# Optimization experiments

Measured on AMD Instinct MI355X. Metric: run time of the kernel, lower is better.

The kernel has to match this reference:

```python
import jax, jax.numpy as jnp
import numpy as np

NUM_HEADS = 8
TAU = 2.0
BN_EPS = 1e-5


def _make_atan_spike(alpha):
    @jax.custom_vjp
    def spike(x):
        return (x >= 0.0).astype(x.dtype)
    def fwd(x):
        return spike(x), x
    def bwd(x, g):
        sg = (alpha / 2.0) / (1.0 + (jnp.pi / 2.0 * alpha * x) ** 2)
        return (g * sg,)
    spike.defvjp(fwd, bwd)
    return spike


def _make_sigmoid_spike(alpha):
    @jax.custom_vjp
    def spike(x):
        return (x >= 0.0).astype(x.dtype)
    def fwd(x):
        return spike(x), x
    def bwd(x, g):
        s = jax.nn.sigmoid(alpha * x)
        return (g * alpha * s * (1.0 - s),)
    spike.defvjp(fwd, bwd)
    return spike

_atan_spike = _make_atan_spike(5.0)       # surrogate.ATan(alpha=5.0)
_sigmoid_spike = _make_sigmoid_spike(4.0)  # spikingjelly default surrogate.Sigmoid(alpha=4.0)


def lif_multistep(x_seq, v_threshold, spike_fn):
    """Multi-step LIF, tau=2, hard reset to 0, detach_reset=True, decay_input=True.
    x_seq: [T, ...]. Returns spike sequence [T, ...]."""
    def step(v, x):
        h = v + (x - v) / TAU
        s = spike_fn(h - v_threshold)
        sd = jax.lax.stop_gradient(s)  # detach_reset
        v_new = h * (1.0 - sd)         # hard reset to v_reset=0
        return v_new, s
    _, s_seq = jax.lax.scan(step, jnp.zeros_like(x_seq[0]), x_seq)
    return s_seq


def bn(x, gamma, beta, mean, var):
    # inference-mode BatchNorm1d over channel dim C of [T,B,C,N]
    inv = gamma / jnp.sqrt(var + BN_EPS)
    return (x - mean[None, None, :, None]) * inv[None, None, :, None] + beta[None, None, :, None]


def setup_inputs() -> dict:
    key = jax.random.key(0)
    T, B, C, H, W = 4, 32, 384, 16, 16
    ks = jax.random.split(key, 20)
    d = {"x": jax.random.normal(ks[0], (T, B, C, H, W), dtype=jnp.float32)}
    std = 1.0 / np.sqrt(C)
    for i, p in enumerate(["q", "k", "proj"]):
        d[p + "_w"] = jax.random.normal(ks[1 + 5 * i], (C, C), dtype=jnp.float32) * std
        d[p + "_gamma"] = jnp.ones((C,), jnp.float32) + 0.1 * jax.random.normal(ks[2 + 5 * i], (C,))
        d[p + "_beta"] = 0.1 * jax.random.normal(ks[3 + 5 * i], (C,))
        d[p + "_mean"] = 0.1 * jax.random.normal(ks[4 + 5 * i], (C,))
        d[p + "_var"] = jax.random.uniform(ks[5 + 5 * i], (C,), minval=0.5, maxval=1.5)
    d["proj_b"] = 0.01 * jax.random.normal(ks[16], (C,))
    return d


def reference(x, q_w, q_gamma, q_beta, q_mean, q_var,
              k_w, k_gamma, k_beta, k_mean, k_var,
              proj_w, proj_gamma, proj_beta, proj_mean, proj_var, proj_b):
    T, B, C, H, W = x.shape
    N = H * W
    Ch = C // NUM_HEADS
    xf = x.reshape(T, B, C, N)

    # q branch: 1x1 conv (C x C matmul) -> BN -> LIF
    q = bn(jnp.einsum('tbcn,dc->tbdn', xf, q_w), q_gamma, q_beta, q_mean, q_var)
    q = lif_multistep(q, 1.0, _atan_spike)
    q = q.reshape(T, B, NUM_HEADS, Ch, N)
    q = jnp.sum(q, axis=3, keepdims=True)          # [T,B,h,1,N]
    attn = lif_multistep(q, 0.5, _sigmoid_spike)    # attn_lif, v_threshold=0.5

    # k branch
    k = bn(jnp.einsum('tbcn,dc->tbdn', xf, k_w), k_gamma, k_beta, k_mean, k_var)
    k = lif_multistep(k, 1.0, _atan_spike)
    k = k.reshape(T, B, NUM_HEADS, Ch, N)

    y = (attn * k).reshape(T, B, C, N)

    # proj: 1x1 conv with bias -> BN -> LIF
    y = jnp.einsum('tbcn,dc->tbdn', y, proj_w) + proj_b[None, None, :, None]
    y = bn(y, proj_gamma, proj_beta, proj_mean, proj_var)
    y = lif_multistep(y, 1.0, _atan_spike)
    return y.reshape(T, B, C, H, W)
```

## Files before the change

### kernel.cpp

```cpp
#include <hip/hip_runtime.h>

typedef _Float16 f16x8 __attribute__((ext_vector_type(8)));
typedef _Float16 f16x4 __attribute__((ext_vector_type(4)));
typedef float    f32x4 __attribute__((ext_vector_type(4)));

#define TT 4
#define BB 32
#define CC 384
#define NN 256

#define WS_X1   25165824
#define WS_WSP  50331648
#define WS_Y    52101120
#define WS_NEED 77266944

__device__ __forceinline__ void async16(void* lds, const void* g) {
    __builtin_amdgcn_global_load_lds(
        (const __attribute__((address_space(1))) unsigned int*)g,
        (__attribute__((address_space(3))) unsigned int*)lds, 16, 0, 0);
}

__global__ __launch_bounds__(256) void wprep(
    const float* __restrict__ qw, const float* __restrict__ kw,
    const float* __restrict__ pw, _Float16* __restrict__ wsp)
{
    int gid = blockIdx.x * 256 + threadIdx.x;
    int which = gid / 36864;
    int e4 = (gid % 36864) * 4;
    const float* src = (which == 0) ? qw : (which == 1) ? kw : pw;
    _Float16* d0 = wsp + (size_t)which * 294912;
    _Float16* d1 = d0 + 147456;
    float4 v = *(const float4*)(src + e4);
    f16x4 h0, h1;
    float vv[4] = {v.x, v.y, v.z, v.w};
#pragma unroll
    for (int j = 0; j < 4; ++j) {
        _Float16 a = (_Float16)vv[j];
        float r = vv[j] - (float)a;
        h0[j] = a; h1[j] = (_Float16)r;
    }
    *(f16x4*)(d0 + e4) = h0;
    *(f16x4*)(d1 + e4) = h1;
}

__global__ __launch_bounds__(256) void xprep(
    const float* __restrict__ x, _Float16* __restrict__ x0,
    _Float16* __restrict__ x1)
{
    __shared__ float xs[64 * 65];
    const int tid = threadIdx.x;
    int bid = blockIdx.x;
    int tb = bid / 24, r = bid % 24;
    int c0 = (r >> 2) * 64, n0 = (r & 3) * 64;

#pragma unroll
    for (int p = 0; p < 4; ++p) {
        int c = (tid >> 4) + p * 16;
        int nl = (tid & 15) * 4;
        float4 v = *(const float4*)&x[((size_t)tb * CC + c0 + c) * NN + n0 + nl];
        *(float4*)&xs[c * 65 + nl] = v;
    }
    __syncthreads();
    int n = tid >> 2, cg = (tid & 3) * 16;
#pragma unroll
    for (int j4 = 0; j4 < 4; ++j4) {
        int c = cg + j4 * 4;
        f16x4 h0, h1;
#pragma unroll
        for (int jj = 0; jj < 4; ++jj) {
            float v = xs[(c + jj) * 65 + n];
            _Float16 a = (_Float16)v;
            float rr = v - (float)a;
            h0[jj] = a; h1[jj] = (_Float16)rr;
        }
        size_t o = ((size_t)tb * NN + n0 + n) * CC + c0 + c;
        *(f16x4*)(x0 + o) = h0;
        *(f16x4*)(x1 + o) = h1;
    }
}

__global__ __launch_bounds__(256, 2) void qk_mfma(
    const _Float16* __restrict__ x0, const _Float16* __restrict__ x1,
    const _Float16* __restrict__ wsp,
    const float* __restrict__ qg, const float* __restrict__ qbe,
    const float* __restrict__ qm, const float* __restrict__ qva,
    const float* __restrict__ kg, const float* __restrict__ kbe,
    const float* __restrict__ km, const float* __restrict__ kva,
    _Float16* __restrict__ y)
{
    __shared__ __align__(16) _Float16 ldsW[12 * 512];

    const int tid  = threadIdx.x;
    const int wave = tid >> 6;
    const int lane = tid & 63;
    const int m16  = lane & 15;
    const int quad = lane >> 4;

    int bid = blockIdx.x;
    int r8 = bid & 7, u = bid >> 3;
    int head = u & 7;
    int s = ((u >> 3) << 3) | r8;
    int b = s >> 1, nh = s & 1;

    const int n0 = nh * 128 + wave * 32;
    const int d0 = head * 48;

    f32x4 vq[3][2], vk[3][2];
    float va[2] = {0.f, 0.f};
#pragma unroll
    for (int dt = 0; dt < 3; ++dt)
#pragma unroll
        for (int nt = 0; nt < 2; ++nt) {
            vq[dt][nt] = (f32x4){0.f, 0.f, 0.f, 0.f};
            vk[dt][nt] = (f32x4){0.f, 0.f, 0.f, 0.f};
        }

    for (int tp = 0; tp < 2; ++tp) {
        f32x4 aq[2][3][2], ak[2][3][2];
#pragma unroll
        for (int t2 = 0; t2 < 2; ++t2)
#pragma unroll
            for (int dt = 0; dt < 3; ++dt)
#pragma unroll
                for (int nt = 0; nt < 2; ++nt) {
                    aq[t2][dt][nt] = (f32x4){0.f, 0.f, 0.f, 0.f};
                    ak[t2][dt][nt] = (f32x4){0.f, 0.f, 0.f, 0.f};
                }

        for (int kc = 0; kc < 12; ++kc) {
            const int c0 = kc * 32;
            __syncthreads();
#pragma unroll
            for (int p = 0; p < 3; ++p) {
                int i = wave + p * 4;
                int brs = i / 3, dt = i % 3;
                const _Float16* gsrc = wsp + (size_t)brs * 147456 +
                    (size_t)(d0 + dt * 16 + m16) * CC + c0 + quad * 8;
                async16(&ldsW[i * 512], gsrc);
            }
            f16x8 bx[2][2][2];
#pragma unroll
            for (int t2 = 0; t2 < 2; ++t2) {
                int t = tp * 2 + t2;
#pragma unroll
                for (int nt = 0; nt < 2; ++nt) {
                    size_t row = ((size_t)(t * BB + b) * NN + n0 + nt * 16 + m16) * CC
                                 + c0 + quad * 8;
                    bx[t2][0][nt] = *(const f16x8*)(x0 + row);
                    bx[t2][1][nt] = *(const f16x8*)(x1 + row);
                }
            }
            __syncthreads();
#pragma unroll
            for (int dt = 0; dt < 3; ++dt) {
                f16x8 wq0 = *(const f16x8*)&ldsW[(0 + dt) * 512 + lane * 8];
                f16x8 wq1 = *(const f16x8*)&ldsW[(3 + dt) * 512 + lane * 8];
                f16x8 wk0 = *(const f16x8*)&ldsW[(6 + dt) * 512 + lane * 8];
                f16x8 wk1 = *(const f16x8*)&ldsW[(9 + dt) * 512 + lane * 8];
#pragma unroll
                for (int t2 = 0; t2 < 2; ++t2)
#pragma unroll
                    for (int nt = 0; nt < 2; ++nt) {
                        f32x4 cq = aq[t2][dt][nt];
                        cq = __builtin_amdgcn_mfma_f32_16x16x32_f16(wq0, bx[t2][0][nt], cq, 0, 0, 0);
                        cq = __builtin_amdgcn_mfma_f32_16x16x32_f16(wq1, bx[t2][0][nt], cq, 0, 0, 0);
                        cq = __builtin_amdgcn_mfma_f32_16x16x32_f16(wq0, bx[t2][1][nt], cq, 0, 0, 0);
                        aq[t2][dt][nt] = cq;
                        f32x4 ck = ak[t2][dt][nt];
                        ck = __builtin_amdgcn_mfma_f32_16x16x32_f16(wk0, bx[t2][0][nt], ck, 0, 0, 0);
                        ck = __builtin_amdgcn_mfma_f32_16x16x32_f16(wk1, bx[t2][0][nt], ck, 0, 0, 0);
                        ck = __builtin_amdgcn_mfma_f32_16x16x32_f16(wk0, bx[t2][1][nt], ck, 0, 0, 0);
                        ak[t2][dt][nt] = ck;
                    }
            }
        }

#pragma unroll
        for (int t2 = 0; t2 < 2; ++t2) {
            int t = tp * 2 + t2;
            float psum[2] = {0.f, 0.f};
            f32x4 ks[3][2];
#pragma unroll
            for (int dt = 0; dt < 3; ++dt) {
                int doff = d0 + dt * 16 + quad * 4;
                f32x4 gq = *(const f32x4*)(qg + doff);
                f32x4 bq = *(const f32x4*)(qbe + doff);
                f32x4 mq = *(const f32x4*)(qm + doff);
                f32x4 vq_ = *(const f32x4*)(qva + doff);
                f32x4 gk_ = *(const f32x4*)(kg + doff);
                f32x4 bk_ = *(const f32x4*)(kbe + doff);
                f32x4 mk_ = *(const f32x4*)(km + doff);
                f32x4 vk_ = *(const f32x4*)(kva + doff);
                float invq[4], invk[4];
#pragma unroll
                for (int rr = 0; rr < 4; ++rr) {
                    invq[rr] = gq[rr] / sqrtf(vq_[rr] + 1e-5f);
                    invk[rr] = gk_[rr] / sqrtf(vk_[rr] + 1e-5f);
                }
#pragma unroll
                for (int nt = 0; nt < 2; ++nt) {
#pragma unroll
                    for (int rr = 0; rr < 4; ++rr) {
                        float bnq = (aq[t2][dt][nt][rr] - mq[rr]) * invq[rr] + bq[rr];
                        float hq  = vq[dt][nt][rr] + (bnq - vq[dt][nt][rr]) * 0.5f;
                        float sq  = (hq - 1.0f >= 0.0f) ? 1.0f : 0.0f;
                        vq[dt][nt][rr] = hq * (1.0f - sq);
                        psum[nt] += sq;
                        float bnk = (ak[t2][dt][nt][rr] - mk_[rr]) * invk[rr] + bk_[rr];
                        float hk  = vk[dt][nt][rr] + (bnk - vk[dt][nt][rr]) * 0.5f;
                        float sk  = (hk - 1.0f >= 0.0f) ? 1.0f : 0.0f;
                        vk[dt][nt][rr] = hk * (1.0f - sk);
                        ks[dt][nt][rr] = sk;
                    }
                }
            }
            float attn[2];
#pragma unroll
            for (int nt = 0; nt < 2; ++nt) {
                float tot = psum[nt];
                tot += __shfl_xor(tot, 16, 64);
                tot += __shfl_xor(tot, 32, 64);
                float ha = va[nt] + (tot - va[nt]) * 0.5f;
                float sa = (ha - 0.5f >= 0.0f) ? 1.0f : 0.0f;
                va[nt] = ha * (1.0f - sa);
                attn[nt] = sa;
            }
#pragma unroll
            for (int dt = 0; dt < 3; ++dt)
#pragma unroll
                for (int nt = 0; nt < 2; ++nt) {
                    f16x4 hv;
#pragma unroll
                    for (int rr = 0; rr < 4; ++rr)
                        hv[rr] = (_Float16)(attn[nt] * ks[dt][nt][rr]);
                    size_t off = ((size_t)(t * BB + b) * NN + n0 + nt * 16 + m16) * CC
                                 + d0 + dt * 16 + quad * 4;
                    *(f16x4*)(y + off) = hv;
                }
        }
    }
}

__global__ __launch_bounds__(128, 2) void proj_mfma(
    const _Float16* __restrict__ y,
    const _Float16* __restrict__ pw0, const _Float16* __restrict__ pw1,
    const float* __restrict__ pg, const float* __restrict__ pbe,
    const float* __restrict__ pm, const float* __restrict__ pva,
    const float* __restrict__ pbias, float* __restrict__ out)
{
    __shared__ __align__(16) _Float16 ldsW[6 * 512];

    const int tid  = threadIdx.x;
    const int wave = tid >> 6;
    const int lane = tid & 63;
    const int m16  = lane & 15;
    const int quad = lane >> 4;

    int bid = blockIdx.x;
    int r8 = bid & 7, u = bid >> 3;
    int dg = u & 7;
    int s = ((u >> 3) << 3) | r8;
    int b = s >> 1, nh = s & 1;

    const int n0 = nh * 128 + wave * 64;
    const int d0 = dg * 48;

    f32x4 vv[3][4];
#pragma unroll
    for (int dt = 0; dt < 3; ++dt)
#pragma unroll
        for (int nt = 0; nt < 4; ++nt) vv[dt][nt] = (f32x4){0.f, 0.f, 0.f, 0.f};

    for (int tp = 0; tp < 2; ++tp) {
        f32x4 acc[2][3][4];
#pragma unroll
        for (int t2 = 0; t2 < 2; ++t2)
#pragma unroll
            for (int dt = 0; dt < 3; ++dt)
#pragma unroll
                for (int nt = 0; nt < 4; ++nt)
                    acc[t2][dt][nt] = (f32x4){0.f, 0.f, 0.f, 0.f};

        for (int kc = 0; kc < 12; ++kc) {
            const int c0 = kc * 32;
            __syncthreads();
#pragma unroll
            for (int p = 0; p < 3; ++p) {
                int i = wave + p * 2;
                int sp = i / 3, dt = i % 3;
                const _Float16* src = (sp ? pw1 : pw0) +
                    (size_t)(d0 + dt * 16 + m16) * CC + c0 + quad * 8;
                async16(&ldsW[i * 512], src);
            }
            f16x8 by[2][4];
#pragma unroll
            for (int t2 = 0; t2 < 2; ++t2) {
                int t = tp * 2 + t2;
#pragma unroll
                for (int nt = 0; nt < 4; ++nt)
                    by[t2][nt] = *(const f16x8*)(y +
                        ((size_t)(t * BB + b) * NN + n0 + nt * 16 + m16) * CC +
                        c0 + quad * 8);
            }
            __syncthreads();
#pragma unroll
            for (int dt = 0; dt < 3; ++dt) {
                f16x8 a0 = *(const f16x8*)&ldsW[(0 + dt) * 512 + lane * 8];
                f16x8 a1 = *(const f16x8*)&ldsW[(3 + dt) * 512 + lane * 8];
#pragma unroll
                for (int t2 = 0; t2 < 2; ++t2)
#pragma unroll
                    for (int nt = 0; nt < 4; ++nt) {
                        f32x4 c = acc[t2][dt][nt];
                        c = __builtin_amdgcn_mfma_f32_16x16x32_f16(a0, by[t2][nt], c, 0, 0, 0);
                        c = __builtin_amdgcn_mfma_f32_16x16x32_f16(a1, by[t2][nt], c, 0, 0, 0);
                        acc[t2][dt][nt] = c;
                    }
            }
        }
#pragma unroll
        for (int t2 = 0; t2 < 2; ++t2) {
            int t = tp * 2 + t2;
#pragma unroll
            for (int dt = 0; dt < 3; ++dt) {
                int doff = d0 + dt * 16 + quad * 4;
                f32x4 g  = *(const f32x4*)(pg + doff);
                f32x4 be = *(const f32x4*)(pbe + doff);
                f32x4 mu = *(const f32x4*)(pm + doff);
                f32x4 va_ = *(const f32x4*)(pva + doff);
                f32x4 bi = *(const f32x4*)(pbias + doff);
                float inv[4];
#pragma unroll
                for (int rr = 0; rr < 4; ++rr)
                    inv[rr] = g[rr] / sqrtf(va_[rr] + 1e-5f);
#pragma unroll
                for (int nt = 0; nt < 4; ++nt) {
#pragma unroll
                    for (int rr = 0; rr < 4; ++rr) {
                        float z  = acc[t2][dt][nt][rr] + bi[rr];
                        float bn = (z - mu[rr]) * inv[rr] + be[rr];
                        float h  = vv[dt][nt][rr] + (bn - vv[dt][nt][rr]) * 0.5f;
                        float sp = (h - 1.0f >= 0.0f) ? 1.0f : 0.0f;
                        vv[dt][nt][rr] = h * (1.0f - sp);
                        out[((size_t)(t * BB + b) * CC + doff + rr) * NN +
                            n0 + nt * 16 + m16] = sp;
                    }
                }
            }
        }
    }
}

#define KC 64
#define LSTR 68
__global__ __launch_bounds__(256) void qk_fused(
    const float* __restrict__ x,
    const float* __restrict__ qw, const float* __restrict__ qg,
    const float* __restrict__ qbe, const float* __restrict__ qm,
    const float* __restrict__ qva,
    const float* __restrict__ kw, const float* __restrict__ kg,
    const float* __restrict__ kbe, const float* __restrict__ km,
    const float* __restrict__ kva,
    unsigned char* __restrict__ y)
{
    __shared__ float xs[KC * LSTR];
    __shared__ float qws[48 * LSTR];
    __shared__ float kws[48 * LSTR];
    __shared__ float hsum[16 * 64];
    const int tid = threadIdx.x, bid = blockIdx.x;
    const int b = bid >> 5, head = (bid >> 2) & 7, n0 = (bid & 3) << 6;
    const int dg = tid >> 4, nl = (tid & 15) << 2;
    float q_inv[3], q_mu[3], q_b[3], k_inv[3], k_mu[3], k_b[3];
#pragma unroll
    for (int i = 0; i < 3; ++i) {
        int d = head * 48 + dg * 3 + i;
        q_inv[i] = qg[d] / sqrtf(qva[d] + 1e-5f); q_mu[i] = qm[d]; q_b[i] = qbe[d];
        k_inv[i] = kg[d] / sqrtf(kva[d] + 1e-5f); k_mu[i] = km[d]; k_b[i] = kbe[d];
    }
    float vq[3][4] = {}, vk[3][4] = {}, va[4] = {};
    for (int t = 0; t < TT; ++t) {
        float accq[3][4] = {}, acck[3][4] = {};
        for (int kc = 0; kc < CC / KC; ++kc) {
            const int c0 = kc * KC;
            __syncthreads();
#pragma unroll
            for (int p = 0; p < 4; ++p) {
                int q4 = tid + p * 256, cc = q4 >> 4, nn = (q4 & 15) << 2;
                *(float4*)&xs[cc * LSTR + nn] =
                    *(const float4*)&x[((size_t)(t * BB + b) * CC + c0 + cc) * NN + n0 + nn];
            }
#pragma unroll
            for (int p = 0; p < 3; ++p) {
                int q4 = tid + p * 256, dl = q4 >> 4, cc = (q4 & 15) << 2;
                *(float4*)&qws[dl * LSTR + cc] = *(const float4*)&qw[(head * 48 + dl) * CC + c0 + cc];
                *(float4*)&kws[dl * LSTR + cc] = *(const float4*)&kw[(head * 48 + dl) * CC + c0 + cc];
            }
            __syncthreads();
#pragma unroll
            for (int cq = 0; cq < KC / 4; ++cq) {
                float xv[4][4];
#pragma unroll
// ... 109 lines not shown
            }
        }
#pragma unroll
        for (int i = 0; i < 4; ++i) {
            float res[4];
#pragma unroll
            for (int j = 0; j < 4; ++j) {
                float z = acc[i][j] + bi[i];
                float bnv = (z - mu[i]) * inv[i] + be[i];
                float h = vvv[i][j] + (bnv - vvv[i][j]) * 0.5f;
                float sx = (h - 1.0f >= 0.0f) ? 1.0f : 0.0f;
                vvv[i][j] = h * (1.0f - sx);
                res[j] = sx;
            }
            *(float4*)&out[((size_t)(t * BB + b) * CC + d0 + dg * 4 + i) * NN + n0 + nl] = *(float4*)&res[0];
        }
    }
}

extern "C" void kernel_launch(void* const* d_in, const int* in_sizes, int n_in,
                              void* d_out, int out_size, void* d_ws, size_t ws_size,
                              hipStream_t stream)
{
    const float* x     = (const float*)d_in[0];
    const float* qw    = (const float*)d_in[1];
    const float* qg    = (const float*)d_in[2];
    const float* qbe   = (const float*)d_in[3];
    const float* qm    = (const float*)d_in[4];
    const float* qva   = (const float*)d_in[5];
    const float* kw    = (const float*)d_in[6];
    const float* kg    = (const float*)d_in[7];
    const float* kbe   = (const float*)d_in[8];
    const float* km    = (const float*)d_in[9];
    const float* kva   = (const float*)d_in[10];
    const float* pw    = (const float*)d_in[11];
    const float* pg    = (const float*)d_in[12];
    const float* pbe   = (const float*)d_in[13];
    const float* pm    = (const float*)d_in[14];
    const float* pva   = (const float*)d_in[15];
    const float* pbias = (const float*)d_in[16];
    float* out = (float*)d_out;

    if (ws_size >= (size_t)WS_NEED) {
        char* w = (char*)d_ws;
        _Float16* x0  = (_Float16*)(w);
        _Float16* x1  = (_Float16*)(w + WS_X1);
        _Float16* wsp = (_Float16*)(w + WS_WSP);
        _Float16* pw0 = wsp + 4 * 147456;
        _Float16* pw1 = wsp + 5 * 147456;
        _Float16* yf  = (_Float16*)(w + WS_Y);

        wprep<<<432, 256, 0, stream>>>(qw, kw, pw, wsp);
        xprep<<<3072, 256, 0, stream>>>(x, x0, x1);
        qk_mfma<<<512, 256, 0, stream>>>(x0, x1, wsp, qg, qbe, qm, qva,
                                         kg, kbe, km, kva, yf);
        proj_mfma<<<512, 128, 0, stream>>>(yf, pw0, pw1, pg, pbe, pm, pva,
                                           pbias, out);
    } else {
        unsigned char* y = (unsigned char*)d_ws;
        qk_fused<<<BB * 8 * (NN / 64), 256, 0, stream>>>(
            x, qw, qg, qbe, qm, qva, kw, kg, kbe, km, kva, y);
        proj_fused<<<BB * (CC / 64) * (NN / 64), 256, 0, stream>>>(
            y, pw, pg, pbe, pm, pva, pbias, out);
    }
}
```

Before: 264.5 us.

## Halve per-wave N tiles in MFMA kernels to double grid and occupancy

Both MFMA kernels now give each wave 16 columns of N instead of 32 or 64, which doubles the grid to 1024 blocks and raises the launch-bounds occupancy hint to 4. The projection kernel also moves to 256 threads and accumulates all four timesteps in a single pass. xprep now writes 8-wide f16 vectors instead of 4-wide. The aim is to cut register pressure and fill more CUs to hide latency, at the cost of each block reusing the LDS-staged weights over fewer columns, so weight-load traffic per FLOP rises.

```diff
diff --git a/kernel.cpp b/kernel.cpp
--- a/kernel.cpp
+++ b/kernel.cpp
@@ -61,25 +61,25 @@
         *(float4*)&xs[c * 65 + nl] = v;
     }
     __syncthreads();
-    int n = tid >> 2, cg = (tid & 3) * 16;
-#pragma unroll
-    for (int j4 = 0; j4 < 4; ++j4) {
-        int c = cg + j4 * 4;
-        f16x4 h0, h1;
-#pragma unroll
-        for (int jj = 0; jj < 4; ++jj) {
-            float v = xs[(c + jj) * 65 + n];
+#pragma unroll
+    for (int p = 0; p < 2; ++p) {
+        int n    = (tid >> 3) + p * 32;
+        int cblk = (tid & 7) * 8;
+        f16x8 h0, h1;
+#pragma unroll
+        for (int jj = 0; jj < 8; ++jj) {
+            float v = xs[(cblk + jj) * 65 + n];
             _Float16 a = (_Float16)v;
-            float rr = v - (float)a;
-            h0[jj] = a; h1[jj] = (_Float16)rr;
-        }
-        size_t o = ((size_t)tb * NN + n0 + n) * CC + c0 + c;
-        *(f16x4*)(x0 + o) = h0;
-        *(f16x4*)(x1 + o) = h1;
-    }
-}
-
-__global__ __launch_bounds__(256, 2) void qk_mfma(
+            h0[jj] = a;
+            h1[jj] = (_Float16)(v - (float)a);
+        }
+        size_t o = ((size_t)tb * NN + n0 + n) * CC + c0 + cblk;
+        *(f16x8*)(x0 + o) = h0;
+        *(f16x8*)(x1 + o) = h1;
+    }
+}
+
+__global__ __launch_bounds__(256, 4) void qk_mfma(
     const _Float16* __restrict__ x0, const _Float16* __restrict__ x1,
     const _Float16* __restrict__ wsp,
     const float* __restrict__ qg, const float* __restrict__ qbe,
@@ -100,32 +100,28 @@
     int r8 = bid & 7, u = bid >> 3;
     int head = u & 7;
     int s = ((u >> 3) << 3) | r8;
-    int b = s >> 1, nh = s & 1;
-
-    const int n0 = nh * 128 + wave * 32;
+    int b = s >> 2, ng = s & 3;
+
+    const int n0 = ng * 64 + wave * 16;
     const int d0 = head * 48;
 
-    f32x4 vq[3][2], vk[3][2];
-    float va[2] = {0.f, 0.f};
-#pragma unroll
-    for (int dt = 0; dt < 3; ++dt)
-#pragma unroll
-        for (int nt = 0; nt < 2; ++nt) {
-            vq[dt][nt] = (f32x4){0.f, 0.f, 0.f, 0.f};
-            vk[dt][nt] = (f32x4){0.f, 0.f, 0.f, 0.f};
-        }
+    f32x4 vq[3], vk[3];
+    float va = 0.f;
+#pragma unroll
+    for (int dt = 0; dt < 3; ++dt) {
+        vq[dt] = (f32x4){0.f, 0.f, 0.f, 0.f};
+        vk[dt] = (f32x4){0.f, 0.f, 0.f, 0.f};
+    }
 
     for (int tp = 0; tp < 2; ++tp) {
-        f32x4 aq[2][3][2], ak[2][3][2];
+        f32x4 aq[2][3], ak[2][3];
 #pragma unroll
         for (int t2 = 0; t2 < 2; ++t2)
 #pragma unroll
-            for (int dt = 0; dt < 3; ++dt)
-#pragma unroll
-                for (int nt = 0; nt < 2; ++nt) {
-                    aq[t2][dt][nt] = (f32x4){0.f, 0.f, 0.f, 0.f};
-                    ak[t2][dt][nt] = (f32x4){0.f, 0.f, 0.f, 0.f};
-                }
+            for (int dt = 0; dt < 3; ++dt) {
+                aq[t2][dt] = (f32x4){0.f, 0.f, 0.f, 0.f};
+                ak[t2][dt] = (f32x4){0.f, 0.f, 0.f, 0.f};
+            }
 
         for (int kc = 0; kc < 12; ++kc) {
             const int c0 = kc * 32;
@@ -138,17 +134,14 @@
                     (size_t)(d0 + dt * 16 + m16) * CC + c0 + quad * 8;
                 async16(&ldsW[i * 512], gsrc);
             }
-            f16x8 bx[2][2][2];
+            f16x8 bx[2][2];
 #pragma unroll
             for (int t2 = 0; t2 < 2; ++t2) {
                 int t = tp * 2 + t2;
-#pragma unroll
-                for (int nt = 0; nt < 2; ++nt) {
-                    size_t row = ((size_t)(t * BB + b) * NN + n0 + nt * 16 + m16) * CC
-                                 + c0 + quad * 8;
-                    bx[t2][0][nt] = *(const f16x8*)(x0 + row);
-                    bx[t2][1][nt] = *(const f16x8*)(x1 + row);
-                }
+                size_t row = ((size_t)(t * BB + b) * NN + n0 + m16) * CC
+                             + c0 + quad * 8;
+                bx[t2][0] = *(const f16x8*)(x0 + row);
+                bx[t2][1] = *(const f16x8*)(x1 + row);
             }
             __syncthreads();
 #pragma unroll
@@ -158,90 +151,74 @@
                 f16x8 wk0 = *(const f16x8*)&ldsW[(6 + dt) * 512 + lane * 8];
                 f16x8 wk1 = *(const f16x8*)&ldsW[(9 + dt) * 512 + lane * 8];
 #pragma unroll
-                for (int t2 = 0; t2 < 2; ++t2)
-#pragma unroll
-                    for (int nt = 0; nt < 2; ++nt) {
-                        f32x4 cq = aq[t2][dt][nt];
-                        cq = __builtin_amdgcn_mfma_f32_16x16x32_f16(wq0, bx[t2][0][nt], cq, 0, 0, 0);
-                        cq = __builtin_amdgcn_mfma_f32_16x16x32_f16(wq1, bx[t2][0][nt], cq, 0, 0, 0);
-                        cq = __builtin_amdgcn_mfma_f32_16x16x32_f16(wq0, bx[t2][1][nt], cq, 0, 0, 0);
-                        aq[t2][dt][nt] = cq;
-                        f32x4 ck = ak[t2][dt][nt];
-                        ck = __builtin_amdgcn_mfma_f32_16x16x32_f16(wk0, bx[t2][0][nt], ck, 0, 0, 0);
-                        ck = __builtin_amdgcn_mfma_f32_16x16x32_f16(wk1, bx[t2][0][nt], ck, 0, 0, 0);
-                        ck = __builtin_amdgcn_mfma_f32_16x16x32_f16(wk0, bx[t2][1][nt], ck, 0, 0, 0);
-                        ak[t2][dt][nt] = ck;
-                    }
+                for (int t2 = 0; t2 < 2; ++t2) {
+                    f32x4 cq = aq[t2][dt];
+                    cq = __builtin_amdgcn_mfma_f32_16x16x32_f16(wq0, bx[t2][0], cq, 0, 0, 0);
+                    cq = __builtin_amdgcn_mfma_f32_16x16x32_f16(wq1, bx[t2][0], cq, 0, 0, 0);
+                    cq = __builtin_amdgcn_mfma_f32_16x16x32_f16(wq0, bx[t2][1], cq, 0, 0, 0);
+                    aq[t2][dt] = cq;
+                    f32x4 ck = ak[t2][dt];
+                    ck = __builtin_amdgcn_mfma_f32_16x16x32_f16(wk0, bx[t2][0], ck, 0, 0, 0);
+                    ck = __builtin_amdgcn_mfma_f32_16x16x32_f16(wk1, bx[t2][0], ck, 0, 0, 0);
+                    ck = __builtin_amdgcn_mfma_f32_16x16x32_f16(wk0, bx[t2][1], ck, 0, 0, 0);
+                    ak[t2][dt] = ck;
+                }
             }
         }
 
 #pragma unroll
         for (int t2 = 0; t2 < 2; ++t2) {
             int t = tp * 2 + t2;
-            float psum[2] = {0.f, 0.f};
-            f32x4 ks[3][2];
+            float psum = 0.f;
+            f32x4 ks[3];
 #pragma unroll
             for (int dt = 0; dt < 3; ++dt) {
                 int doff = d0 + dt * 16 + quad * 4;
-                f32x4 gq = *(const f32x4*)(qg + doff);
-                f32x4 bq = *(const f32x4*)(qbe + doff);
-                f32x4 mq = *(const f32x4*)(qm + doff);
+                f32x4 gq  = *(const f32x4*)(qg + doff);
+                f32x4 bq  = *(const f32x4*)(qbe + doff);
+                f32x4 mq  = *(const f32x4*)(qm + doff);
                 f32x4 vq_ = *(const f32x4*)(qva + doff);
                 f32x4 gk_ = *(const f32x4*)(kg + doff);
                 f32x4 bk_ = *(const f32x4*)(kbe + doff);
                 f32x4 mk_ = *(const f32x4*)(km + doff);
                 f32x4 vk_ = *(const f32x4*)(kva + doff);
-                float invq[4], invk[4];
 #pragma unroll
                 for (int rr = 0; rr < 4; ++rr) {
-                    invq[rr] = gq[rr] / sqrtf(vq_[rr] + 1e-5f);
-                    invk[rr] = gk_[rr] / sqrtf(vk_[rr] + 1e-5f);
+                    float invq = gq[rr] / sqrtf(vq_[rr] + 1e-5f);
+                    float invk = gk_[rr] / sqrtf(vk_[rr] + 1e-5f);
+                    float bnq = (aq[t2][dt][rr] - mq[rr]) * invq + bq[rr];
+                    float hq  = vq[dt][rr] + (bnq - vq[dt][rr]) * 0.5f;
+                    float sq  = (hq - 1.0f >= 0.0f) ? 1.0f : 0.0f;
+                    vq[dt][rr] = hq * (1.0f - sq);
+                    psum += sq;
+                    float bnk = (ak[t2][dt][rr] - mk_[rr]) * invk + bk_[rr];
+                    float hk  = vk[dt][rr] + (bnk - vk[dt][rr]) * 0.5f;
+                    float sk  = (hk - 1.0f >= 0.0f) ? 1.0f : 0.0f;
+                    vk[dt][rr] = hk * (1.0f - sk);
+                    ks[dt][rr] = sk;
                 }
-#pragma unroll
-                for (int nt = 0; nt < 2; ++nt) {
-#pragma unroll
-                    for (int rr = 0; rr < 4; ++rr) {
-                        float bnq = (aq[t2][dt][nt][rr] - mq[rr]) * invq[rr] + bq[rr];
-                        float hq  = vq[dt][nt][rr] + (bnq - vq[dt][nt][rr]) * 0.5f;
-                        float sq  = (hq - 1.0f >= 0.0f) ? 1.0f : 0.0f;
-                        vq[dt][nt][rr] = hq * (1.0f - sq);
-                        psum[nt] += sq;
-                        float bnk = (ak[t2][dt][nt][rr] - mk_[rr]) * invk[rr] + bk_[rr];
-                        float hk  = vk[dt][nt][rr] + (bnk - vk[dt][nt][rr]) * 0.5f;
-                        float sk  = (hk - 1.0f >= 0.0f) ? 1.0f : 0.0f;
-                        vk[dt][nt][rr] = hk * (1.0f - sk);
-                        ks[dt][nt][rr] = sk;
-                    }
-                }
-            }
-            float attn[2];
-#pragma unroll
-            for (int nt = 0; nt < 2; ++nt) {
-                float tot = psum[nt];
-                tot += __shfl_xor(tot, 16, 64);
-                tot += __shfl_xor(tot, 32, 64);
-                float ha = va[nt] + (tot - va[nt]) * 0.5f;
-                float sa = (ha - 0.5f >= 0.0f) ? 1.0f : 0.0f;
-                va[nt] = ha * (1.0f - sa);
-                attn[nt] = sa;
-            }
-#pragma unroll
-            for (int dt = 0; dt < 3; ++dt)
-#pragma unroll
-                for (int nt = 0; nt < 2; ++nt) {
-                    f16x4 hv;
-#pragma unroll
-                    for (int rr = 0; rr < 4; ++rr)
-                        hv[rr] = (_Float16)(attn[nt] * ks[dt][nt][rr]);
-                    size_t off = ((size_t)(t * BB + b) * NN + n0 + nt * 16 + m16) * CC
-                                 + d0 + dt * 16 + quad * 4;
-                    *(f16x4*)(y + off) = hv;
-                }
-        }
-    }
-}
-
-__global__ __launch_bounds__(128, 2) void proj_mfma(
+            }
+            psum += __shfl_xor(psum, 16, 64);
+            psum += __shfl_xor(psum, 32, 64);
+            float ha = va + (psum - va) * 0.5f;
+            float sa = (ha - 0.5f >= 0.0f) ? 1.0f : 0.0f;
+            va = ha * (1.0f - sa);
+            float attn = sa;
+#pragma unroll
+            for (int dt = 0; dt < 3; ++dt) {
+                f16x4 hv;
+#pragma unroll
+                for (int rr = 0; rr < 4; ++rr)
+                    hv[rr] = (_Float16)(attn * ks[dt][rr]);
+                size_t off = ((size_t)(t * BB + b) * NN + n0 + m16) * CC
+                             + d0 + dt * 16 + quad * 4;
+                *(f16x4*)(y + off) = hv;
+            }
+        }
+    }
+}
+
+__global__ __launch_bounds__(256, 4) void proj_mfma(
     const _Float16* __restrict__ y,
     const _Float16* __restrict__ pw0, const _Float16* __restrict__ pw1,
     const float* __restrict__ pg, const float* __restrict__ pbe,
@@ -260,92 +237,76 @@
     int r8 = bid & 7, u = bid >> 3;
     int dg = u & 7;
     int s = ((u >> 3) << 3) | r8;
-    int b = s >> 1, nh = s & 1;
-
-    const int n0 = nh * 128 + wave * 64;
+    int b = s >> 2, ng = s & 3;
+
+    const int n0 = ng * 64 + wave * 16;
     const int d0 = dg * 48;
 
-    f32x4 vv[3][4];
-#pragma unroll
-    for (int dt = 0; dt < 3; ++dt)
-#pragma unroll
-        for (int nt = 0; nt < 4; ++nt) vv[dt][nt] = (f32x4){0.f, 0.f, 0.f, 0.f};
-
-    for (int tp = 0; tp < 2; ++tp) {
-        f32x4 acc[2][3][4];
-#pragma unroll
-        for (int t2 = 0; t2 < 2; ++t2)
-#pragma unroll
-            for (int dt = 0; dt < 3; ++dt)
-#pragma unroll
-                for (int nt = 0; nt < 4; ++nt)
-                    acc[t2][dt][nt] = (f32x4){0.f, 0.f, 0.f, 0.f};
-
-        for (int kc = 0; kc < 12; ++kc) {
-            const int c0 = kc * 32;
-            __syncthreads();
-#pragma unroll
-            for (int p = 0; p < 3; ++p) {
-                int i = wave + p * 2;
+    f32x4 vv[3];
+#pragma unroll
+    for (int dt = 0; dt < 3; ++dt) vv[dt] = (f32x4){0.f, 0.f, 0.f, 0.f};
+
+    f32x4 acc[4][3];
+#pragma unroll
+    for (int t = 0; t < 4; ++t)
+#pragma unroll
+        for (int dt = 0; dt < 3; ++dt)
+            acc[t][dt] = (f32x4){0.f, 0.f, 0.f, 0.f};
+
+    for (int kc = 0; kc < 12; ++kc) {
+        const int c0 = kc * 32;
+        __syncthreads();
+#pragma unroll
+        for (int p = 0; p < 2; ++p) {
+            int i = wave + p * 4;
+            if (i < 6) {
                 int sp = i / 3, dt = i % 3;
                 const _Float16* src = (sp ? pw1 : pw0) +
                     (size_t)(d0 + dt * 16 + m16) * CC + c0 + quad * 8;
                 async16(&ldsW[i * 512], src);
             }
-            f16x8 by[2][4];
-#pragma unroll
-            for (int t2 = 0; t2 < 2; ++t2) {
-                int t = tp * 2 + t2;
-#pragma unroll
-                for (int nt = 0; nt < 4; ++nt)
-                    by[t2][nt] = *(const f16x8*)(y +
-                        ((size_t)(t * BB + b) * NN + n0 + nt * 16 + m16) * CC +
-                        c0 + quad * 8);
-            }
-            __syncthreads();
-#pragma unroll
-            for (int dt = 0; dt < 3; ++dt) {
-                f16x8 a0 = *(const f16x8*)&ldsW[(0 + dt) * 512 + lane * 8];
-                f16x8 a1 = *(const f16x8*)&ldsW[(3 + dt) * 512 + lane * 8];
-#pragma unroll
-                for (int t2 = 0; t2 < 2; ++t2)
-#pragma unroll
-                    for (int nt = 0; nt < 4; ++nt) {
-                        f32x4 c = acc[t2][dt][nt];
-                        c = __builtin_amdgcn_mfma_f32_16x16x32_f16(a0, by[t2][nt], c, 0, 0, 0);
-                        c = __builtin_amdgcn_mfma_f32_16x16x32_f16(a1, by[t2][nt], c, 0, 0, 0);
-                        acc[t2][dt][nt] = c;
-                    }
-            }
-        }
-#pragma unroll
-        for (int t2 = 0; t2 < 2; ++t2) {
-            int t = tp * 2 + t2;
-#pragma unroll
-            for (int dt = 0; dt < 3; ++dt) {
-                int doff = d0 + dt * 16 + quad * 4;
-                f32x4 g  = *(const f32x4*)(pg + doff);
-                f32x4 be = *(const f32x4*)(pbe + doff);
-                f32x4 mu = *(const f32x4*)(pm + doff);
-                f32x4 va_ = *(const f32x4*)(pva + doff);
-                f32x4 bi = *(const f32x4*)(pbias + doff);
-                float inv[4];
-#pragma unroll
-                for (int rr = 0; rr < 4; ++rr)
-                    inv[rr] = g[rr] / sqrtf(va_[rr] + 1e-5f);
-#pragma unroll
-                for (int nt = 0; nt < 4; ++nt) {
-#pragma unroll
-                    for (int rr = 0; rr < 4; ++rr) {
-                        float z  = acc[t2][dt][nt][rr] + bi[rr];
-                        float bn = (z - mu[rr]) * inv[rr] + be[rr];
-                        float h  = vv[dt][nt][rr] + (bn - vv[dt][nt][rr]) * 0.5f;
-                        float sp = (h - 1.0f >= 0.0f) ? 1.0f : 0.0f;
-                        vv[dt][nt][rr] = h * (1.0f - sp);
-                        out[((size_t)(t * BB + b) * CC + doff + rr) * NN +
-                            n0 + nt * 16 + m16] = sp;
-                    }
-                }
+        }
+        f16x8 by[4];
+#pragma unroll
+        for (int t = 0; t < 4; ++t)
+            by[t] = *(const f16x8*)(y +
+                ((size_t)(t * BB + b) * NN + n0 + m16) * CC + c0 + quad * 8);
+        __syncthreads();
+#pragma unroll
+        for (int dt = 0; dt < 3; ++dt) {
+            f16x8 a0 = *(const f16x8*)&ldsW[(0 + dt) * 512 + lane * 8];
+            f16x8 a1 = *(const f16x8*)&ldsW[(3 + dt) * 512 + lane * 8];
+#pragma unroll
+            for (int t = 0; t < 4; ++t) {
+                f32x4 c = acc[t][dt];
+                c = __builtin_amdgcn_mfma_f32_16x16x32_f16(a0, by[t], c, 0, 0, 0);
+                c = __builtin_amdgcn_mfma_f32_16x16x32_f16(a1, by[t], c, 0, 0, 0);
+                acc[t][dt] = c;
+            }
+        }
+    }
+#pragma unroll
+    for (int dt = 0; dt < 3; ++dt) {
+        int doff = d0 + dt * 16 + quad * 4;
+        f32x4 g   = *(const f32x4*)(pg + doff);
+        f32x4 be  = *(const f32x4*)(pbe + doff);
+        f32x4 mu  = *(const f32x4*)(pm + doff);
+        f32x4 va_ = *(const f32x4*)(pva + doff);
+        f32x4 bi  = *(const f32x4*)(pbias + doff);
+        float inv[4];
+#pragma unroll
+        for (int rr = 0; rr < 4; ++rr)
+            inv[rr] = g[rr] / sqrtf(va_[rr] + 1e-5f);
+#pragma unroll
+        for (int t = 0; t < 4; ++t) {
+#pragma unroll
+            for (int rr = 0; rr < 4; ++rr) {
+                float z  = acc[t][dt][rr] + bi[rr];
+                float bn = (z - mu[rr]) * inv[rr] + be[rr];
+                float h  = vv[dt][rr] + (bn - vv[dt][rr]) * 0.5f;
+                float sp = (h - 1.0f >= 0.0f) ? 1.0f : 0.0f;
+                vv[dt][rr] = h * (1.0f - sp);
+                out[((size_t)(t * BB + b) * CC + doff + rr) * NN + n0 + m16] = sp;
             }
         }
     }
@@ -562,10 +523,10 @@
 
         wprep<<<432, 256, 0, stream>>>(qw, kw, pw, wsp);
         xprep<<<3072, 256, 0, stream>>>(x, x0, x1);
-        qk_mfma<<<512, 256, 0, stream>>>(x0, x1, wsp, qg, qbe, qm, qva,
-                                         kg, kbe, km, kva, yf);
-        proj_mfma<<<512, 128, 0, stream>>>(yf, pw0, pw1, pg, pbe, pm, pva,
-                                           pbias, out);
+        qk_mfma<<<1024, 256, 0, stream>>>(x0, x1, wsp, qg, qbe, qm, qva,
+                                          kg, kbe, km, kva, yf);
+        proj_mfma<<<1024, 256, 0, stream>>>(yf, pw0, pw1, pg, pbe, pm, pva,
+                                            pbias, out);
     } else {
         unsigned char* y = (unsigned char*)d_ws;
         qk_fused<<<BB * 8 * (NN / 64), 256, 0, stream>>>(
```

After: 311.8 us. 17.9% more time.

## Drop LDS weight staging and remap qk/proj MFMA tiles per wave

Applied to the files above, without the earlier changes.

Both MFMA kernels stop staging weights through LDS and drop their __syncthreads barriers; each wave now loads its weight fragments straight from global memory. qk_mfma assigns one head per wave over a 32-column n slab. The intermediate y is written with a permuted channel order inside each head so stores are contiguous, and wprep permutes the proj weight columns to match. proj_mfma now uses 256 threads and accumulates all four timesteps in one pass, and xprep writes 8-wide f16 vectors. The aim is to remove barrier and LDS overhead and improve store coalescing, at the cost of redundant global weight reads (relying on cache) and higher register pressure in proj.

```diff
diff --git a/kernel.cpp b/kernel.cpp
--- a/kernel.cpp
+++ b/kernel.cpp
@@ -14,33 +14,45 @@
 #define WS_Y    52101120
 #define WS_NEED 77266944
 
-__device__ __forceinline__ void async16(void* lds, const void* g) {
-    __builtin_amdgcn_global_load_lds(
-        (const __attribute__((address_space(1))) unsigned int*)g,
-        (__attribute__((address_space(3))) unsigned int*)lds, 16, 0, 0);
-}
-
 __global__ __launch_bounds__(256) void wprep(
     const float* __restrict__ qw, const float* __restrict__ kw,
     const float* __restrict__ pw, _Float16* __restrict__ wsp)
 {
     int gid = blockIdx.x * 256 + threadIdx.x;
-    int which = gid / 36864;
-    int e4 = (gid % 36864) * 4;
-    const float* src = (which == 0) ? qw : (which == 1) ? kw : pw;
-    _Float16* d0 = wsp + (size_t)which * 294912;
-    _Float16* d1 = d0 + 147456;
-    float4 v = *(const float4*)(src + e4);
-    f16x4 h0, h1;
-    float vv[4] = {v.x, v.y, v.z, v.w};
-#pragma unroll
-    for (int j = 0; j < 4; ++j) {
-        _Float16 a = (_Float16)vv[j];
-        float r = vv[j] - (float)a;
-        h0[j] = a; h1[j] = (_Float16)r;
-    }
-    *(f16x4*)(d0 + e4) = h0;
-    *(f16x4*)(d1 + e4) = h1;
+    if (gid < 73728) {
+        int which = gid / 36864;
+        int e4 = (gid % 36864) * 4;
+        const float* src = which ? kw : qw;
+        _Float16* d0 = wsp + (size_t)which * 294912;
+        _Float16* d1 = d0 + 147456;
+        float4 v = *(const float4*)(src + e4);
+        float vv[4] = {v.x, v.y, v.z, v.w};
+        f16x4 h0, h1;
+#pragma unroll
+        for (int j = 0; j < 4; ++j) {
+            _Float16 a = (_Float16)vv[j];
+            h0[j] = a; h1[j] = (_Float16)(vv[j] - (float)a);
+        }
+        *(f16x4*)(d0 + e4) = h0;
+        *(f16x4*)(d1 + e4) = h1;
+    } else {
+        int pid = gid - 73728;
+        int e4 = pid * 4;
+        int d = e4 / 384, p4 = e4 % 384;
+        int h = p4 / 48, w = p4 % 48;
+        int quad = w / 12, slot = (w % 12) >> 2;
+        _Float16* wp0 = wsp + 4 * 147456;
+        _Float16* wp1 = wsp + 5 * 147456;
+        f16x4 h0, h1;
+#pragma unroll
+        for (int j = 0; j < 4; ++j) {
+            float v = pw[d * CC + h * 48 + slot * 16 + quad * 4 + j];
+            _Float16 a = (_Float16)v;
+            h0[j] = a; h1[j] = (_Float16)(v - (float)a);
+        }
+        *(f16x4*)(wp0 + e4) = h0;
+        *(f16x4*)(wp1 + e4) = h1;
+    }
 }
 
 __global__ __launch_bounds__(256) void xprep(
@@ -61,21 +73,21 @@
         *(float4*)&xs[c * 65 + nl] = v;
     }
     __syncthreads();
-    int n = tid >> 2, cg = (tid & 3) * 16;
-#pragma unroll
-    for (int j4 = 0; j4 < 4; ++j4) {
-        int c = cg + j4 * 4;
-        f16x4 h0, h1;
-#pragma unroll
-        for (int jj = 0; jj < 4; ++jj) {
-            float v = xs[(c + jj) * 65 + n];
+#pragma unroll
+    for (int p = 0; p < 2; ++p) {
+        int n    = (tid >> 3) + p * 32;
+        int cblk = (tid & 7) * 8;
+        f16x8 h0, h1;
+#pragma unroll
+        for (int jj = 0; jj < 8; ++jj) {
+            float v = xs[(cblk + jj) * 65 + n];
             _Float16 a = (_Float16)v;
-            float rr = v - (float)a;
-            h0[jj] = a; h1[jj] = (_Float16)rr;
-        }
-        size_t o = ((size_t)tb * NN + n0 + n) * CC + c0 + c;
-        *(f16x4*)(x0 + o) = h0;
-        *(f16x4*)(x1 + o) = h1;
+            h0[jj] = a;
+            h1[jj] = (_Float16)(v - (float)a);
+        }
+        size_t o = ((size_t)tb * NN + n0 + n) * CC + c0 + cblk;
+        *(f16x8*)(x0 + o) = h0;
+        *(f16x8*)(x1 + o) = h1;
     }
 }
 
@@ -88,22 +100,27 @@
     const float* __restrict__ km, const float* __restrict__ kva,
     _Float16* __restrict__ y)
 {
-    __shared__ __align__(16) _Float16 ldsW[12 * 512];
-
     const int tid  = threadIdx.x;
     const int wave = tid >> 6;
     const int lane = tid & 63;
     const int m16  = lane & 15;
     const int quad = lane >> 4;
 
-    int bid = blockIdx.x;
-    int r8 = bid & 7, u = bid >> 3;
-    int head = u & 7;
-    int s = ((u >> 3) << 3) | r8;
-    int b = s >> 1, nh = s & 1;
-
-    const int n0 = nh * 128 + wave * 32;
-    const int d0 = head * 48;
+    int bid  = blockIdx.x;
+    int xcd  = bid & 7;
+    int hh   = (bid >> 3) & 1;
+    int s    = bid >> 4;
+    int slab = s * 8 + xcd;
+    int b    = slab >> 3;
+    int nb   = (slab & 7) * 32;
+
+    const int head = hh * 4 + wave;
+    const int d0   = head * 48;
+
+    const _Float16* wq0 = wsp;
+    const _Float16* wq1 = wsp + 147456;
+    const _Float16* wk0 = wsp + 2 * 147456;
+    const _Float16* wk1 = wsp + 3 * 147456;
 
     f32x4 vq[3][2], vk[3][2];
     float va[2] = {0.f, 0.f};
@@ -129,47 +146,38 @@
 
         for (int kc = 0; kc < 12; ++kc) {
             const int c0 = kc * 32;
-            __syncthreads();
-#pragma unroll
-            for (int p = 0; p < 3; ++p) {
-                int i = wave + p * 4;
-                int brs = i / 3, dt = i % 3;
-                const _Float16* gsrc = wsp + (size_t)brs * 147456 +
-                    (size_t)(d0 + dt * 16 + m16) * CC + c0 + quad * 8;
-                async16(&ldsW[i * 512], gsrc);
-            }
             f16x8 bx[2][2][2];
 #pragma unroll
             for (int t2 = 0; t2 < 2; ++t2) {
                 int t = tp * 2 + t2;
 #pragma unroll
                 for (int nt = 0; nt < 2; ++nt) {
-                    size_t row = ((size_t)(t * BB + b) * NN + n0 + nt * 16 + m16) * CC
-                                 + c0 + quad * 8;
+                    size_t row = ((size_t)(t * BB + b) * NN + nb + nt * 16 + m16)
+                                 * CC + c0 + quad * 8;
                     bx[t2][0][nt] = *(const f16x8*)(x0 + row);
                     bx[t2][1][nt] = *(const f16x8*)(x1 + row);
                 }
             }
-            __syncthreads();
 #pragma unroll
             for (int dt = 0; dt < 3; ++dt) {
-                f16x8 wq0 = *(const f16x8*)&ldsW[(0 + dt) * 512 + lane * 8];
-                f16x8 wq1 = *(const f16x8*)&ldsW[(3 + dt) * 512 + lane * 8];
-                f16x8 wk0 = *(const f16x8*)&ldsW[(6 + dt) * 512 + lane * 8];
-                f16x8 wk1 = *(const f16x8*)&ldsW[(9 + dt) * 512 + lane * 8];
+                size_t wrow = (size_t)(d0 + dt * 16 + m16) * CC + c0 + quad * 8;
+                f16x8 q0 = *(const f16x8*)(wq0 + wrow);
+                f16x8 q1 = *(const f16x8*)(wq1 + wrow);
+                f16x8 k0 = *(const f16x8*)(wk0 + wrow);
+                f16x8 k1 = *(const f16x8*)(wk1 + wrow);
 #pragma unroll
                 for (int t2 = 0; t2 < 2; ++t2)
 #pragma unroll
                     for (int nt = 0; nt < 2; ++nt) {
                         f32x4 cq = aq[t2][dt][nt];
-                        cq = __builtin_amdgcn_mfma_f32_16x16x32_f16(wq0, bx[t2][0][nt], cq, 0, 0, 0);
-                        cq = __builtin_amdgcn_mfma_f32_16x16x32_f16(wq1, bx[t2][0][nt], cq, 0, 0, 0);
-                        cq = __builtin_amdgcn_mfma_f32_16x16x32_f16(wq0, bx[t2][1][nt], cq, 0, 0, 0);
+                        cq = __builtin_amdgcn_mfma_f32_16x16x32_f16(q0, bx[t2][0][nt], cq, 0, 0, 0);
+                        cq = __builtin_amdgcn_mfma_f32_16x16x32_f16(q1, bx[t2][0][nt], cq, 0, 0, 0);
+                        cq = __builtin_amdgcn_mfma_f32_16x16x32_f16(q0, bx[t2][1][nt], cq, 0, 0, 0);
                         aq[t2][dt][nt] = cq;
                         f32x4 ck = ak[t2][dt][nt];
-                        ck = __builtin_amdgcn_mfma_f32_16x16x32_f16(wk0, bx[t2][0][nt], ck, 0, 0, 0);
-                        ck = __builtin_amdgcn_mfma_f32_16x16x32_f16(wk1, bx[t2][0][nt], ck, 0, 0, 0);
-                        ck = __builtin_amdgcn_mfma_f32_16x16x32_f16(wk0, bx[t2][1][nt], ck, 0, 0, 0);
+                        ck = __builtin_amdgcn_mfma_f32_16x16x32_f16(k0, bx[t2][0][nt], ck, 0, 0, 0);
+                        ck = __builtin_amdgcn_mfma_f32_16x16x32_f16(k1, bx[t2][0][nt], ck, 0, 0, 0);
+                        ck = __builtin_amdgcn_mfma_f32_16x16x32_f16(k0, bx[t2][1][nt], ck, 0, 0, 0);
                         ak[t2][dt][nt] = ck;
                     }
             }
@@ -183,30 +191,26 @@
 #pragma unroll
             for (int dt = 0; dt < 3; ++dt) {
                 int doff = d0 + dt * 16 + quad * 4;
-                f32x4 gq = *(const f32x4*)(qg + doff);
-                f32x4 bq = *(const f32x4*)(qbe + doff);
-                f32x4 mq = *(const f32x4*)(qm + doff);
+                f32x4 gq  = *(const f32x4*)(qg + doff);
+                f32x4 bq  = *(const f32x4*)(qbe + doff);
+                f32x4 mq  = *(const f32x4*)(qm + doff);
                 f32x4 vq_ = *(const f32x4*)(qva + doff);
                 f32x4 gk_ = *(const f32x4*)(kg + doff);
                 f32x4 bk_ = *(const f32x4*)(kbe + doff);
                 f32x4 mk_ = *(const f32x4*)(km + doff);
                 f32x4 vk_ = *(const f32x4*)(kva + doff);
-                float invq[4], invk[4];
 #pragma unroll
                 for (int rr = 0; rr < 4; ++rr) {
-                    invq[rr] = gq[rr] / sqrtf(vq_[rr] + 1e-5f);
-                    invk[rr] = gk_[rr] / sqrtf(vk_[rr] + 1e-5f);
-                }
-#pragma unroll
-                for (int nt = 0; nt < 2; ++nt) {
-#pragma unroll
-                    for (int rr = 0; rr < 4; ++rr) {
-                        float bnq = (aq[t2][dt][nt][rr] - mq[rr]) * invq[rr] + bq[rr];
+                    float invq = gq[rr] / sqrtf(vq_[rr] + 1e-5f);
+                    float invk = gk_[rr] / sqrtf(vk_[rr] + 1e-5f);
+#pragma unroll
+                    for (int nt = 0; nt < 2; ++nt) {
+                        float bnq = (aq[t2][dt][nt][rr] - mq[rr]) * invq + bq[rr];
                         float hq  = vq[dt][nt][rr] + (bnq - vq[dt][nt][rr]) * 0.5f;
                         float sq  = (hq - 1.0f >= 0.0f) ? 1.0f : 0.0f;
                         vq[dt][nt][rr] = hq * (1.0f - sq);
                         psum[nt] += sq;
-                        float bnk = (ak[t2][dt][nt][rr] - mk_[rr]) * invk[rr] + bk_[rr];
+                        float bnk = (ak[t2][dt][nt][rr] - mk_[rr]) * invk + bk_[rr];
                         float hk  = vk[dt][nt][rr] + (bnk - vk[dt][nt][rr]) * 0.5f;
                         float sk  = (hk - 1.0f >= 0.0f) ? 1.0f : 0.0f;
                         vk[dt][nt][rr] = hk * (1.0f - sk);
@@ -214,7 +218,6 @@
                     }
                 }
             }
-            float attn[2];
 #pragma unroll
             for (int nt = 0; nt < 2; ++nt) {
                 float tot = psum[nt];
@@ -223,130 +226,111 @@
                 float ha = va[nt] + (tot - va[nt]) * 0.5f;
                 float sa = (ha - 0.5f >= 0.0f) ? 1.0f : 0.0f;
                 va[nt] = ha * (1.0f - sa);
-                attn[nt] = sa;
-            }
-#pragma unroll
-            for (int dt = 0; dt < 3; ++dt)
-#pragma unroll
-                for (int nt = 0; nt < 2; ++nt) {
+                float attn = sa;
+                size_t yrow = ((size_t)(t * BB + b) * NN + nb + nt * 16 + m16)
+                              * CC + d0 + quad * 12;
+#pragma unroll
+                for (int dt = 0; dt < 3; ++dt) {
                     f16x4 hv;
 #pragma unroll
                     for (int rr = 0; rr < 4; ++rr)
-                        hv[rr] = (_Float16)(attn[nt] * ks[dt][nt][rr]);
-                    size_t off = ((size_t)(t * BB + b) * NN + n0 + nt * 16 + m16) * CC
-                                 + d0 + dt * 16 + quad * 4;
-                    *(f16x4*)(y + off) = hv;
-                }
-        }
-    }
-}
-
-__global__ __launch_bounds__(128, 2) void proj_mfma(
+                        hv[rr] = (_Float16)(attn * ks[dt][nt][rr]);
+                    *(f16x4*)(y + yrow + dt * 4) = hv;
+                }
+            }
+        }
+    }
+}
+
+__global__ __launch_bounds__(256, 2) void proj_mfma(
     const _Float16* __restrict__ y,
     const _Float16* __restrict__ pw0, const _Float16* __restrict__ pw1,
     const float* __restrict__ pg, const float* __restrict__ pbe,
     const float* __restrict__ pm, const float* __restrict__ pva,
     const float* __restrict__ pbias, float* __restrict__ out)
 {
-    __shared__ __align__(16) _Float16 ldsW[6 * 512];
-
     const int tid  = threadIdx.x;
     const int wave = tid >> 6;
     const int lane = tid & 63;
     const int m16  = lane & 15;
     const int quad = lane >> 4;
 
-    int bid = blockIdx.x;
-    int r8 = bid & 7, u = bid >> 3;
-    int dg = u & 7;
-    int s = ((u >> 3) << 3) | r8;
-    int b = s >> 1, nh = s & 1;
-
-    const int n0 = nh * 128 + wave * 64;
-    const int d0 = dg * 48;
-
-    f32x4 vv[3][4];
+    int bid  = blockIdx.x;
+    int xcd  = bid & 7;
+    int dgg  = (bid >> 3) & 1;
+    int s    = bid >> 4;
+    int slab = s * 8 + xcd;
+    int b    = slab >> 3;
+    int nb   = (slab & 7) * 32;
+    const int d0w = dgg * 192 + wave * 48;
+
+    f32x4 vv[3][2];
 #pragma unroll
     for (int dt = 0; dt < 3; ++dt)
 #pragma unroll
-        for (int nt = 0; nt < 4; ++nt) vv[dt][nt] = (f32x4){0.f, 0.f, 0.f, 0.f};
-
-    for (int tp = 0; tp < 2; ++tp) {
-        f32x4 acc[2][3][4];
-#pragma unroll
-        for (int t2 = 0; t2 < 2; ++t2)
-#pragma unroll
-            for (int dt = 0; dt < 3; ++dt)
-#pragma unroll
-                for (int nt = 0; nt < 4; ++nt)
-                    acc[t2][dt][nt] = (f32x4){0.f, 0.f, 0.f, 0.f};
-
-        for (int kc = 0; kc < 12; ++kc) {
-            const int c0 = kc * 32;
-            __syncthreads();
-#pragma unroll
-            for (int p = 0; p < 3; ++p) {
-                int i = wave + p * 2;
-                int sp = i / 3, dt = i % 3;
-                const _Float16* src = (sp ? pw1 : pw0) +
-                    (size_t)(d0 + dt * 16 + m16) * CC + c0 + quad * 8;
-                async16(&ldsW[i * 512], src);
-            }
-            f16x8 by[2][4];
-#pragma unroll
-            for (int t2 = 0; t2 < 2; ++t2) {
-                int t = tp * 2 + t2;
-#pragma unroll
-                for (int nt = 0; nt < 4; ++nt)
-                    by[t2][nt] = *(const f16x8*)(y +
-                        ((size_t)(t * BB + b) * NN + n0 + nt * 16 + m16) * CC +
-                        c0 + quad * 8);
-            }
-            __syncthreads();
-#pragma unroll
-            for (int dt = 0; dt < 3; ++dt) {
-                f16x8 a0 = *(const f16x8*)&ldsW[(0 + dt) * 512 + lane * 8];
-                f16x8 a1 = *(const f16x8*)&ldsW[(3 + dt) * 512 + lane * 8];
-#pragma unroll
-                for (int t2 = 0; t2 < 2; ++t2)
-#pragma unroll
-                    for (int nt = 0; nt < 4; ++nt) {
-                        f32x4 c = acc[t2][dt][nt];
-                        c = __builtin_amdgcn_mfma_f32_16x16x32_f16(a0, by[t2][nt], c, 0, 0, 0);
-                        c = __builtin_amdgcn_mfma_f32_16x16x32_f16(a1, by[t2][nt], c, 0, 0, 0);
-                        acc[t2][dt][nt] = c;
-                    }
-            }
-        }
-#pragma unroll
-        for (int t2 = 0; t2 < 2; ++t2) {
-            int t = tp * 2 + t2;
-#pragma unroll
-            for (int dt = 0; dt < 3; ++dt) {
-                int doff = d0 + dt * 16 + quad * 4;
-                f32x4 g  = *(const f32x4*)(pg + doff);
-                f32x4 be = *(const f32x4*)(pbe + doff);
-                f32x4 mu = *(const f32x4*)(pm + doff);
-                f32x4 va_ = *(const f32x4*)(pva + doff);
-                f32x4 bi = *(const f32x4*)(pbias + doff);
-                float inv[4];
-#pragma unroll
-                for (int rr = 0; rr < 4; ++rr)
-                    inv[rr] = g[rr] / sqrtf(va_[rr] + 1e-5f);
-#pragma unroll
-                for (int nt = 0; nt < 4; ++nt) {
-#pragma unroll
-                    for (int rr = 0; rr < 4; ++rr) {
-                        float z  = acc[t2][dt][nt][rr] + bi[rr];
-                        float bn = (z - mu[rr]) * inv[rr] + be[rr];
-                        float h  = vv[dt][nt][rr] + (bn - vv[dt][nt][rr]) * 0.5f;
-                        float sp = (h - 1.0f >= 0.0f) ? 1.0f : 0.0f;
-                        vv[dt][nt][rr] = h * (1.0f - sp);
-                        out[((size_t)(t * BB + b) * CC + doff + rr) * NN +
-                            n0 + nt * 16 + m16] = sp;
-                    }
-                }
-            }
+        for (int nt = 0; nt < 2; ++nt) vv[dt][nt] = (f32x4){0.f, 0.f, 0.f, 0.f};
+
+    f32x4 acc[4][3][2];
+#pragma unroll
+    for (int t = 0; t < 4; ++t)
+#pragma unroll
+        for (int dt = 0; dt < 3; ++dt)
+#pragma unroll
+            for (int nt = 0; nt < 2; ++nt)
+                acc[t][dt][nt] = (f32x4){0.f, 0.f, 0.f, 0.f};
+
+    for (int kc = 0; kc < 12; ++kc) {
+        const int c0 = kc * 32;
+        f16x8 by[4][2];
+#pragma unroll
+        for (int t = 0; t < 4; ++t)
+#pragma unroll
+            for (int nt = 0; nt < 2; ++nt)
+                by[t][nt] = *(const f16x8*)(y +
+                    ((size_t)(t * BB + b) * NN + nb + nt * 16 + m16) * CC +
+                    c0 + quad * 8);
+#pragma unroll
+        for (int dt = 0; dt < 3; ++dt) {
+            size_t wrow = (size_t)(d0w + dt * 16 + m16) * CC + c0 + quad * 8;
+            f16x8 a0 = *(const f16x8*)(pw0 + wrow);
+            f16x8 a1 = *(const f16x8*)(pw1 + wrow);
+#pragma unroll
+            for (int t = 0; t < 4; ++t)
+#pragma unroll
+                for (int nt = 0; nt < 2; ++nt) {
+                    f32x4 c = acc[t][dt][nt];
+                    c = __builtin_amdgcn_mfma_f32_16x16x32_f16(a0, by[t][nt], c, 0, 0, 0);
+                    c = __builtin_amdgcn_mfma_f32_16x16x32_f16(a1, by[t][nt], c, 0, 0, 0);
+                    acc[t][dt][nt] = c;
+                }
+        }
+    }
+#pragma unroll
+    for (int dt = 0; dt < 3; ++dt) {
+        int doff = d0w + dt * 16 + quad * 4;
+        f32x4 g   = *(const f32x4*)(pg + doff);
+        f32x4 be  = *(const f32x4*)(pbe + doff);
+        f32x4 mu  = *(const f32x4*)(pm + doff);
+        f32x4 va_ = *(const f32x4*)(pva + doff);
+        f32x4 bi  = *(const f32x4*)(pbias + doff);
+        float inv[4];
+#pragma unroll
+        for (int rr = 0; rr < 4; ++rr)
+            inv[rr] = g[rr] / sqrtf(va_[rr] + 1e-5f);
+#pragma unroll
+        for (int t = 0; t < 4; ++t) {
+#pragma unroll
+            for (int nt = 0; nt < 2; ++nt)
+#pragma unroll
+                for (int rr = 0; rr < 4; ++rr) {
+                    float z  = acc[t][dt][nt][rr] + bi[rr];
+                    float bn = (z - mu[rr]) * inv[rr] + be[rr];
+                    float h  = vv[dt][nt][rr] + (bn - vv[dt][nt][rr]) * 0.5f;
+                    float sp = (h - 1.0f >= 0.0f) ? 1.0f : 0.0f;
+                    vv[dt][nt][rr] = h * (1.0f - sp);
+                    out[((size_t)(t * BB + b) * CC + doff + rr) * NN +
+                        nb + nt * 16 + m16] = sp;
+                }
         }
     }
 }
@@ -564,7 +548,7 @@
         xprep<<<3072, 256, 0, stream>>>(x, x0, x1);
         qk_mfma<<<512, 256, 0, stream>>>(x0, x1, wsp, qg, qbe, qm, qva,
                                          kg, kbe, km, kva, yf);
-        proj_mfma<<<512, 128, 0, stream>>>(yf, pw0, pw1, pg, pbe, pm, pva,
+        proj_mfma<<<512, 256, 0, stream>>>(yf, pw0, pw1, pg, pbe, pm, pva,
                                            pbias, out);
     } else {
         unsigned char* y = (unsigned char*)d_ws;
```

Measured after the change: 300.3 us. 1.14x slower.
